# Kernel tuning notes

Hardware: AMD Instinct MI355X
Metric: run time of the kernel (lower is better)

Reference implementation:

```python
import jax, jax.numpy as jnp
import numpy as np

B, S, HID, NH = 2, 2048, 1024, 16
HD = HID // NH  # head_dim = 64


def setup_inputs() -> dict:
    key = jax.random.key(0)
    ks = jax.random.split(key, 9)
    init = 0.02
    return {
        "x": jax.random.normal(ks[0], (B, S, HID), dtype=jnp.float32),
        "Wq": jax.random.normal(ks[1], (HID, HID), dtype=jnp.float32) * init,
        "bq": jnp.zeros((HID,), dtype=jnp.float32),
        "Wk": jax.random.normal(ks[2], (HID, HID), dtype=jnp.float32) * init,
        "bk": jnp.zeros((HID,), dtype=jnp.float32),
        "Wv": jax.random.normal(ks[3], (HID, HID), dtype=jnp.float32) * init,
        "bv": jnp.zeros((HID,), dtype=jnp.float32),
        "Wo": jax.random.normal(ks[4], (HID, HID), dtype=jnp.float32) * init,
        "bo": jnp.zeros((HID,), dtype=jnp.float32),
    }


def _split_heads(t):
    # [B, S, HID] -> [B, NH, S, HD]
    return t.reshape(B, S, NH, HD).transpose(0, 2, 1, 3)


def reference(x, Wq, bq, Wk, bk, Wv, bv, Wo, bo):
    q = _split_heads(x @ Wq.T + bq)
    k = _split_heads(x @ Wk.T + bk)
    v = _split_heads(x @ Wv.T + bv)

    # Faithful to source: scores = QK^T / (head_dim ** -0.5) == QK^T * sqrt(head_dim)
    inv_scale = jnp.asarray(HD ** (-0.5), dtype=x.dtype)
    scores = jnp.einsum("bhqd,bhkd->bhqk", q, k) / inv_scale

    causal_mask = jnp.triu(jnp.ones((S, S), dtype=bool), k=1)  # True above diagonal
    scores = jnp.where(causal_mask, jnp.asarray(-jnp.inf, dtype=scores.dtype), scores)
    attn = jax.nn.softmax(scores, axis=-1)  # dropout = identity (eval mode)

    ctx = jnp.einsum("bhqk,bhkd->bhqd", attn, v)
    ctx = ctx.transpose(0, 2, 1, 3).reshape(B, S, HID)
    out = ctx @ Wo.T + bo  # out_layer Linear; dropout = identity
    return out, attn
```

## Files before the change

### kernel.cpp

```cpp
#include <hip/hip_runtime.h>
#include <hip/hip_bf16.h>

#define BB   2
#define SS   2048
#define HID  1024
#define NH   16
#define HD   64
#define NEGS -30000.0f

typedef __bf16 bf16x8 __attribute__((ext_vector_type(8)));
typedef __bf16 bf16x4 __attribute__((ext_vector_type(4)));
typedef float  f32x4  __attribute__((ext_vector_type(4)));

static __device__ __forceinline__ f32x4 mfma_bf16(bf16x8 a, bf16x8 b, f32x4 c) {
    return __builtin_amdgcn_mfma_f32_16x16x32_bf16(a, b, c, 0, 0, 0);
}

static __device__ __forceinline__ void split_bf16(float f, __bf16* hp, __bf16* lp) {
    __bf16 h = (__bf16)f;
    *hp = h;
    *lp = (__bf16)(f - (float)h);
}

static __device__ __forceinline__ float clampf(float v, float lo, float hi) {
    return fminf(fmaxf(v, lo), hi);
}

static __device__ __forceinline__ void gll16(const __bf16* g, __bf16* l) {
    __builtin_amdgcn_global_load_lds((const void*)g, (void*)l, 16, 0, 0);
}

static __device__ __forceinline__ void barrier_lds() {
    asm volatile("s_waitcnt lgkmcnt(0)" ::: "memory");
    __builtin_amdgcn_sched_barrier(0);
    __builtin_amdgcn_s_barrier();
    __builtin_amdgcn_sched_barrier(0);
}

static __device__ __forceinline__ void barrier_vm4() {
    asm volatile("s_waitcnt vmcnt(4) lgkmcnt(0)" ::: "memory");
    __builtin_amdgcn_sched_barrier(0);
    __builtin_amdgcn_s_barrier();
    __builtin_amdgcn_sched_barrier(0);
}
static __device__ __forceinline__ void barrier_vm0() {
    asm volatile("s_waitcnt vmcnt(0) lgkmcnt(0)" ::: "memory");
    __builtin_amdgcn_sched_barrier(0);
    __builtin_amdgcn_s_barrier();
    __builtin_amdgcn_sched_barrier(0);
}

__global__ __launch_bounds__(256) void split_kernel(
    const float* __restrict__ x,
    const float* __restrict__ Wq, const float* __restrict__ Wk,
    const float* __restrict__ Wv, const float* __restrict__ Wo,
    __bf16* __restrict__ xh, __bf16* __restrict__ xl,
    __bf16* __restrict__ wqh, __bf16* __restrict__ wql,
    __bf16* __restrict__ wkh, __bf16* __restrict__ wkl,
    __bf16* __restrict__ wvh, __bf16* __restrict__ woh)
{
    const int bid = blockIdx.x;
    if (bid < 4096) {
        const int i4 = bid * 256 + threadIdx.x;
        const float4 v = ((const float4*)x)[i4];
        const float* p = (const float*)&v;
        bf16x4 h4, l4v;
#pragma unroll
        for (int j = 0; j < 4; j++) { __bf16 hh, ll; split_bf16(p[j], &hh, &ll); h4[j] = hh; l4v[j] = ll; }
        *(bf16x4*)&xh[(size_t)i4 * 4] = h4;
        *(bf16x4*)&xl[(size_t)i4 * 4] = l4v;
        return;
    }
    const int wb = bid - 4096;
    const int which = (wb >> 10) + 1;
    const int i4 = (wb & 1023) * 256 + threadIdx.x;
    const float* src = which == 1 ? Wq : which == 2 ? Wk : which == 3 ? Wv : Wo;
    const float sc = (which == 1) ? 8.0f : 1.0f;
    const float4 v = ((const float4*)src)[i4];
    const float* p = (const float*)&v;
    bf16x4 h4, l4v;
#pragma unroll
    for (int j = 0; j < 4; j++) { __bf16 hh, ll; split_bf16(p[j] * sc, &hh, &ll); h4[j] = hh; l4v[j] = ll; }
    if (which == 1)      { *(bf16x4*)&wqh[(size_t)i4 * 4] = h4; *(bf16x4*)&wql[(size_t)i4 * 4] = l4v; }
    else if (which == 2) { *(bf16x4*)&wkh[(size_t)i4 * 4] = h4; *(bf16x4*)&wkl[(size_t)i4 * 4] = l4v; }
    else if (which == 3) { *(bf16x4*)&wvh[(size_t)i4 * 4] = h4; }
    else                 { *(bf16x4*)&woh[(size_t)i4 * 4] = h4; }
}

__global__ __launch_bounds__(256) void qkv_kernel(
    const __bf16* __restrict__ xh, const __bf16* __restrict__ xl,
    const __bf16* __restrict__ wqh, const __bf16* __restrict__ wql,
    const __bf16* __restrict__ wkh, const __bf16* __restrict__ wkl,
    const __bf16* __restrict__ wvh,
    const float* __restrict__ bq, const float* __restrict__ bk, const float* __restrict__ bv,
    __bf16* __restrict__ qh, __bf16* __restrict__ ql,
    __bf16* __restrict__ kh, __bf16* __restrict__ kl,
    __bf16* __restrict__ vt)
{
    __shared__ __align__(16) __bf16 smem[32768];

    const int stream = blockIdx.x >> 3, ct = blockIdx.x & 7;
    const int t0 = blockIdx.y * 128, c0 = ct * 128;
    const bool qk = stream < 2;
    const __bf16* const Bhg = stream == 0 ? wqh : stream == 1 ? wkh : wvh;
    const __bf16* const Blg = stream == 0 ? wql : wkl;
    const float* const bias = stream == 0 ? bq : stream == 1 ? bk : bv;
    const float bscale = stream == 0 ? 8.0f : 1.0f;

    const int tid = threadIdx.x, wave = tid >> 6, lane = tid & 63;
    const int l16 = lane & 15, quad = lane >> 4;
    const int wr = wave >> 1, wc = wave & 1;

    const int ar0 = tid >> 2,         as0 = (tid & 3) ^ (ar0 & 3);
    const int ar1 = (256 + tid) >> 2, as1 = ((256 + tid) & 3) ^ (ar1 & 3);
    const size_t aoff0 = (size_t)(t0 + ar0) * HID + as0 * 8;
    const size_t aoff1 = (size_t)(t0 + ar1) * HID + as1 * 8;
    const size_t boff0 = (size_t)(c0 + ar0) * HID + as0 * 8;
    const size_t boff1 = (size_t)(c0 + ar1) * HID + as1 * 8;
    const int ld0 = wave << 9, ld1 = (4 + wave) << 9;

#define QKV_STAGE(b_, k0_) do {                                   \
        __bf16* s_ = smem + (b_) * 16384;                         \
        gll16(xh + aoff0 + (k0_), s_ + ld0);                      \
        gll16(xh + aoff1 + (k0_), s_ + ld1);                      \
        gll16(Bhg + boff0 + (k0_), s_ + 8192 + ld0);              \
        gll16(Bhg + boff1 + (k0_), s_ + 8192 + ld1);              \
        if (qk) {                                                 \
            gll16(xl + aoff0 + (k0_), s_ + 4096 + ld0);           \
            gll16(xl + aoff1 + (k0_), s_ + 4096 + ld1);           \
            gll16(Blg + boff0 + (k0_), s_ + 12288 + ld0);         \
            gll16(Blg + boff1 + (k0_), s_ + 12288 + ld1);         \
        }                                                         \
    } while (0)

    const f32x4 zero4 = {0.f, 0.f, 0.f, 0.f};
    f32x4 acc[4][4];
#pragma unroll
    for (int i = 0; i < 4; i++)
#pragma unroll
        for (int j = 0; j < 4; j++) acc[i][j] = zero4;

    QKV_STAGE(0, 0);
    for (int k0 = 0; k0 < HID; k0 += 32) {
        const int cur = (k0 >> 5) & 1;
        __syncthreads();
        if (k0 + 32 < HID) QKV_STAGE(cur ^ 1, k0 + 32);
        __bf16* const s_ = smem + cur * 16384;

        bf16x8 aH[4], aL[4], bHf[4], bLf[4];
#pragma unroll
        for (int mf = 0; mf < 4; mf++) {
            const int row = wr * 64 + mf * 16 + l16;
            const int off = row * 32 + ((quad ^ (row & 3)) << 3);
            aH[mf] = *(const bf16x8*)(s_ + off);
            if (qk) aL[mf] = *(const bf16x8*)(s_ + 4096 + off);
        }
#pragma unroll
        for (int nf = 0; nf < 4; nf++) {
            const int row = wc * 64 + nf * 16 + l16;
            const int off = row * 32 + ((quad ^ (row & 3)) << 3);
            bHf[nf] = *(const bf16x8*)(s_ + 8192 + off);
            if (qk) bLf[nf] = *(const bf16x8*)(s_ + 12288 + off);
        }
#pragma unroll
        for (int mf = 0; mf < 4; mf++)
#pragma unroll
            for (int nf = 0; nf < 4; nf++) {
                acc[mf][nf] = mfma_bf16(aH[mf], bHf[nf], acc[mf][nf]);
                if (qk) {
                    acc[mf][nf] = mfma_bf16(aH[mf], bLf[nf], acc[mf][nf]);
                    acc[mf][nf] = mfma_bf16(aL[mf], bHf[nf], acc[mf][nf]);
                }
            }
    }
#undef QKV_STAGE

    const int bidx = t0 >> 11;
    const int s0 = t0 & (SS - 1);

    if (qk) {
        __bf16* const Es = smem;
        __bf16* const hi_arr = stream == 0 ? qh : kh;
        __bf16* const lo_arr = stream == 0 ? ql : kl;
#pragma unroll
        for (int pass = 0; pass < 2; pass++) {
            __syncthreads();
#pragma unroll
            for (int nf = 0; nf < 4; nf++) {
                const int dcl = wc * 64 + nf * 16 + l16;
                const float bv_ = bias[c0 + dcl] * bscale;
#pragma unroll
                for (int mf = 0; mf < 4; mf++)
#pragma unroll
                    for (int r = 0; r < 4; r++) {
                        const int srl = wr * 64 + mf * 16 + quad * 4 + r;
                        const float v = clampf(acc[mf][nf][r] + bv_, -1e4f, 1e4f);
                        __bf16 hv, lv;
                        split_bf16(v, &hv, &lv);
                        Es[srl * 132 + dcl] = pass ? lv : hv;
                    }
            }
            __syncthreads();
            __bf16* const dst = pass ? lo_arr : hi_arr;
#pragma unroll
            for (int i = 0; i < 8; i++) {
                const int idx = tid + i * 256;
                const int row = idx >> 4, c16 = idx & 15;
                const int hh = (c0 >> 6) + (c16 >> 3);
                const int dd = (c16 & 7) * 8;
                const size_t o = ((size_t)(bidx * NH + hh) * SS + (s0 + row)) * HD + dd;
                *(uint4*)&dst[o] = *(const uint4*)&Es[row * 132 + c16 * 8];
            }
        }
    } else {
        __syncthreads();
        __bf16* const Vts = smem + wave * 4608;
#pragma unroll
        for (int nf = 0; nf < 4; nf++) {
            const int dloc = nf * 16 + l16;
            const float bv_ = bias[c0 + wc * 64 + dloc];
#pragma unroll
            for (int mf = 0; mf < 4; mf++)
#pragma unroll
                for (int r = 0; r < 4; r++)
                    Vts[dloc * 72 + mf * 16 + quad * 4 + r] =
                        (__bf16)clampf(acc[mf][nf][r] + bv_, -1e4f, 1e4f);
        }
        const int hh = (c0 + wc * 64) >> 6;
        const size_t vb = (size_t)(bidx * NH + hh) * HD * SS;
        const int sc0 = s0 + wr * 64;
#pragma unroll
        for (int j = 0; j < 8; j++) {
            const int idx = j * 64 + lane;
            const int d = idx >> 3, c8 = idx & 7;
            *(uint4*)&vt[vb + (size_t)d * SS + sc0 + c8 * 8] =
                *(const uint4*)&Vts[d * 72 + c8 * 8];
        }
    }
}

__global__ __launch_bounds__(512, 4) void attn_kernel(
    const __bf16* __restrict__ qh, const __bf16* __restrict__ ql,
    const __bf16* __restrict__ kh, const __bf16* __restrict__ kl,
    const __bf16* __restrict__ vt,
    float* __restrict__ attn, __bf16* __restrict__ ctx)
{
    __shared__ __align__(16) __bf16 Kh0[4096], Kl0[4096], Kh1[4096], Kl1[4096];
    __shared__ __align__(16) __bf16 Vt0[4096], Vt1[4096];
    __shared__ __align__(16) __bf16 Ps[128][72];

    const int bid  = blockIdx.x;
    const int half = bid >> 8;
    const int ii   = bid & 255;
    const int g    = ii & 7;
    const int bh   = g + 8 * ((ii >> 3) & 3);
    const int p    = ii >> 5;
    const int qt   = half ? p : (15 - p);
    const int nj   = 2 * qt + 2;
    const int b    = bh >> 4, h = bh & 15;

    const int tid  = threadIdx.x;
    const int wave = tid >> 6, lane = tid & 63;
    const int l16  = lane & 15, quad = lane >> 4;

    const int sr = tid >> 3, ssw = (tid & 7) ^ (sr & 7);
    const size_t kq = (size_t)sr * HD + ssw * 8;
    const size_t vq = (size_t)sr * SS + ssw * 8;
    const int ldw = wave << 9;

    const __bf16* const khp = kh + (size_t)bh * SS * HD;
    const __bf16* const klp = kl + (size_t)bh * SS * HD;
    const __bf16* const vtp = vt + (size_t)bh * HD * SS;

#define STAGE_K(j_, KH, KL) do {                                  \
        const __bf16* kg_ = khp + (size_t)(j_) * (64 * HD);       \
        const __bf16* lg_ = klp + (size_t)(j_) * (64 * HD);       \
        gll16(kg_ + kq, (KH) + ldw); gll16(lg_ + kq, (KL) + ldw); \
    } while (0)
#define STAGE_V(j_, VT) do {                                      \
        const __bf16* vg_ = vtp + (size_t)(j_) * 64;              \
        gll16(vg_ + vq, (VT) + ldw);                              \
    } while (0)

    const f32x4 zero4 = {0.f, 0.f, 0.f, 0.f};

    bf16x8 aHq[2], aLq[2];
    {
        const size_t qrow = ((size_t)bh * SS + qt * 128 + wave * 16 + l16) * HD;
#pragma unroll
        for (int ks = 0; ks < 2; ks++) {
            aHq[ks] = *(const bf16x8*)&qh[qrow + ks * 32 + quad * 8];
            aLq[ks] = *(const bf16x8*)&ql[qrow + ks * 32 + quad * 8];
        }
    }

    float m4[4], l4[4];
#pragma unroll
    for (int r = 0; r < 4; r++) { m4[r] = NEGS; l4[r] = 0.f; }

    STAGE_K(0, Kh0, Kl0);
    __syncthreads();

    for (int j = 0; j < nj; j++) {
        if (j) __syncthreads();
        if (j < nj - 1) {
            if (j & 1) STAGE_K(j + 1, Kh0, Kl0);
            else       STAGE_K(j + 1, Kh1, Kl1);
        }
        const __bf16* const Khc = (j & 1) ? Kh1 : Kh0;
        const __bf16* const Klc = (j & 1) ? Kl1 : Kl0;

        f32x4 sacc[4] = {zero4, zero4, zero4, zero4};
#pragma unroll
        for (int ks = 0; ks < 2; ks++)
#pragma unroll
            for (int c = 0; c < 4; c++) {
                const int krow = c * 16 + l16;
                const int ko = krow * 64 + (((ks * 4 + quad) ^ (krow & 7)) << 3);
                const bf16x8 bH = *(const bf16x8*)(Khc + ko);
                const bf16x8 bL = *(const bf16x8*)(Klc + ko);
                sacc[c] = mfma_bf16(aHq[ks], bH, sacc[c]);
                sacc[c] = mfma_bf16(aHq[ks], bL, sacc[c]);
                sacc[c] = mfma_bf16(aLq[ks], bH, sacc[c]);
            }
        if (j >= 2 * qt) {
            const int cb = j * 64, qr = qt * 128 + wave * 16 + quad * 4;
#pragma unroll
            for (int c = 0; c < 4; c++) {
                const int col = cb + c * 16 + l16;
#pragma unroll
                for (int r = 0; r < 4; r++)
                    if (col > qr + r) sacc[c][r] = NEGS;
            }
        }
#pragma unroll
        for (int r = 0; r < 4; r++) {
            const float mx = fmaxf(fmaxf(sacc[0][r], sacc[1][r]),
                                   fmaxf(sacc[2][r], sacc[3][r]));
            const float mn = fmaxf(m4[r], mx);
            l4[r] = l4[r] * __expf(m4[r] - mn)
                  + __expf(sacc[0][r] - mn) + __expf(sacc[1][r] - mn)
                  + __expf(sacc[2][r] - mn) + __expf(sacc[3][r] - mn);
            m4[r] = mn;
        }
    }

    float il[4];
#pragma unroll
    for (int r = 0; r < 4; r++) {
#pragma unroll
        for (int off = 1; off < 16; off <<= 1) {
            const float mo  = __shfl_xor(m4[r], off);
            const float lo_ = __shfl_xor(l4[r], off);
            const float mn  = fmaxf(m4[r], mo);
            l4[r] = l4[r] * __expf(m4[r] - mn) + lo_ * __expf(mo - mn);
            m4[r] = mn;
        }
        il[r] = (l4[r] > 0.f) ? (1.0f / l4[r]) : 0.f;
    }

    f32x4 cacc[4] = {zero4, zero4, zero4, zero4};

    __syncthreads();
    STAGE_K(0, Kh0, Kl0);
    STAGE_V(0, Vt0);

    for (int j = 0; j < nj; j++) {
        if (j == 0) barrier_vm0();
        else        barrier_vm4();
        if (j < nj - 1) {
            if (j & 1) { STAGE_K(j + 1, Kh0, Kl0); STAGE_V(j + 1, Vt0); }
            else       { STAGE_K(j + 1, Kh1, Kl1); STAGE_V(j + 1, Vt1); }
        }
        const __bf16* const Khc = (j & 1) ? Kh1 : Kh0;
        const __bf16* const Klc = (j & 1) ? Kl1 : Kl0;
        const __bf16* const Vtc = (j & 1) ? Vt1 : Vt0;

        f32x4 sacc[4] = {zero4, zero4, zero4, zero4};
#pragma unroll
        for (int ks = 0; ks < 2; ks++)
#pragma unroll
            for (int c = 0; c < 4; c++) {
                const int krow = c * 16 + l16;
                const int ko = krow * 64 + (((ks * 4 + quad) ^ (krow & 7)) << 3);
                const bf16x8 bH = *(const bf16x8*)(Khc + ko);
                const bf16x8 bL = *(const bf16x8*)(Klc + ko);
                sacc[c] = mfma_bf16(aHq[ks], bH, sacc[c]);
                sacc[c] = mfma_bf16(aHq[ks], bL, sacc[c]);
                sacc[c] = mfma_bf16(aLq[ks], bH, sacc[c]);
            }
        if (j >= 2 * qt) {
            const int cb = j * 64, qr = qt * 128 + wave * 16 + quad * 4;
#pragma unroll
            for (int c = 0; c < 4; c++) {
                const int col = cb + c * 16 + l16;
#pragma unroll
                for (int r = 0; r < 4; r++)
                    if (col > qr + r) sacc[c][r] = NEGS;
            }
        }
#pragma unroll
        for (int c = 0; c < 4; c++)
#pragma unroll
            for (int r = 0; r < 4; r++) {
                const float pv = clampf(__expf(sacc[c][r] - m4[r]) * il[r], 0.f, 1.f);
                Ps[wave * 16 + quad * 4 + r][c * 16 + l16] = (__bf16)pv;
            }
        barrier_lds();

#pragma unroll
        for (int i = 0; i < 2; i++) {
            const int idx = tid + i * 512;
            const int row = idx >> 3, c8 = idx & 7;
            const size_t o = ((size_t)bh * SS + qt * 128 + row) * SS + j * 64 + c8 * 8;
            __bf16 tmp[8];
            *(uint4*)tmp = *(const uint4*)&Ps[row][c8 * 8];
            float4 f0, f1;
            f0.x = (float)tmp[0]; f0.y = (float)tmp[1];
            f0.z = (float)tmp[2]; f0.w = (float)tmp[3];
            f1.x = (float)tmp[4]; f1.y = (float)tmp[5];
            f1.z = (float)tmp[6]; f1.w = (float)tmp[7];
            *(float4*)&attn[o]     = f0;
            *(float4*)&attn[o + 4] = f1;
        }
#pragma unroll
        for (int ks = 0; ks < 2; ks++) {
            const bf16x8 ap = *(const bf16x8*)&Ps[wave * 16 + l16][ks * 32 + quad * 8];
#pragma unroll
            for (int dt = 0; dt < 4; dt++) {
                const int vrow = dt * 16 + l16;
                const int vo = vrow * 64 + (((ks * 4 + quad) ^ (vrow & 7)) << 3);
                cacc[dt] = mfma_bf16(ap, *(const bf16x8*)(Vtc + vo), cacc[dt]);
            }
        }
    }

    const float4 zf4 = {0.f, 0.f, 0.f, 0.f};
    for (int j = nj; j < SS / 64; j++) {
#pragma unroll
        for (int i = 0; i < 4; i++) {
            const int idx = tid + i * 512;
            const int row = idx >> 4, c4 = idx & 15;
            const size_t o = ((size_t)bh * SS + qt * 128 + row) * SS + j * 64 + c4 * 4;
            *(float4*)&attn[o] = zf4;
        }
    }

    __syncthreads();
#pragma unroll
    for (int dt = 0; dt < 4; dt++) {
        const int d = dt * 16 + l16;
#pragma unroll
        for (int r = 0; r < 4; r++)
            Ps[wave * 16 + quad * 4 + r][d] =
                (__bf16)clampf(cacc[dt][r], -1e4f, 1e4f);
    }
    __syncthreads();
#pragma unroll
    for (int i = 0; i < 2; i++) {
        const int idx = tid + i * 512;
        const int row = idx >> 3, c8 = idx & 7;
        *(uint4*)&ctx[(size_t)(b * SS + qt * 128 + row) * HID + h * 64 + c8 * 8] =
            *(const uint4*)&Ps[row][c8 * 8];
    }
#undef STAGE_K
#undef STAGE_V
}

__global__ __launch_bounds__(256) void out_kernel(
    const __bf16* __restrict__ ctx, const __bf16* __restrict__ woh,
    const float* __restrict__ bo, float* __restrict__ out)
{
    __shared__ __align__(16) __bf16 smem[12288];

    const int o0 = blockIdx.x * 64;
    const int t0 = blockIdx.y * 128;

    const int tid = threadIdx.x, wave = tid >> 6, lane = tid & 63;
    const int l16 = lane & 15, quad = lane >> 4;
    const int wr = wave >> 1, wc = wave & 1;

    const int ar0 = tid >> 2,         as0 = (tid & 3) ^ (ar0 & 3);
    const int ar1 = (256 + tid) >> 2, as1 = ((256 + tid) & 3) ^ (ar1 & 3);
    const size_t aoff0 = (size_t)(t0 + ar0) * HID + as0 * 8;
    const size_t aoff1 = (size_t)(t0 + ar1) * HID + as1 * 8;
    const size_t boff  = (size_t)(o0 + ar0) * HID + as0 * 8;
    const int ld0 = wave << 9, ld1 = (4 + wave) << 9;

#define OUT_STAGE(b_, k0_) do {                                   \
        __bf16* s_ = smem + (b_) * 6144;                          \
        gll16(ctx + aoff0 + (k0_), s_ + ld0);                     \
        gll16(ctx + aoff1 + (k0_), s_ + ld1);                     \
        gll16(woh + boff + (k0_), s_ + 4096 + ld0);               \
    } while (0)

    const f32x4 zero4 = {0.f, 0.f, 0.f, 0.f};
    f32x4 acc[4][2];
#pragma unroll
    for (int i = 0; i < 4; i++)
#pragma unroll
        for (int j = 0; j < 2; j++) acc[i][j] = zero4;

    OUT_STAGE(0, 0);
    for (int k0 = 0; k0 < HID; k0 += 32) {
        const int cur = (k0 >> 5) & 1;
        __syncthreads();
        if (k0 + 32 < HID) OUT_STAGE(cur ^ 1, k0 + 32);
        __bf16* const s_ = smem + cur * 6144;

        bf16x8 aH[4], bHf[2];
#pragma unroll
        for (int mf = 0; mf < 4; mf++) {
            const int row = wr * 64 + mf * 16 + l16;
            aH[mf] = *(const bf16x8*)(s_ + row * 32 + ((quad ^ (row & 3)) << 3));
        }
#pragma unroll
        for (int nf = 0; nf < 2; nf++) {
            const int row = wc * 32 + nf * 16 + l16;
            bHf[nf] = *(const bf16x8*)(s_ + 4096 + row * 32 + ((quad ^ (row & 3)) << 3));
        }
#pragma unroll
        for (int mf = 0; mf < 4; mf++)
#pragma unroll
            for (int nf = 0; nf < 2; nf++)
                acc[mf][nf] = mfma_bf16(aH[mf], bHf[nf], acc[mf][nf]);
    }
#undef OUT_STAGE

#pragma unroll
    for (int nf = 0; nf < 2; nf++) {
        const int dcol = o0 + wc * 32 + nf * 16 + l16;
        const float bias = bo[dcol];
#pragma unroll
        for (int mf = 0; mf < 4; mf++)
#pragma unroll
            for (int r = 0; r < 4; r++) {
                const int t = t0 + wr * 64 + mf * 16 + quad * 4 + r;
                out[(size_t)t * HID + dcol] = clampf(acc[mf][nf][r] + bias, -1e4f, 1e4f);
            }
    }
}

extern "C" void kernel_launch(void* const* d_in, const int* in_sizes, int n_in,
                              void* d_out, int out_size, void* d_ws, size_t ws_size,
                              hipStream_t stream) {
    const float* x  = (const float*)d_in[0];
    const float* Wq = (const float*)d_in[1];
    const float* bq = (const float*)d_in[2];
    const float* Wk = (const float*)d_in[3];
    const float* bk = (const float*)d_in[4];
    const float* Wv = (const float*)d_in[5];
    const float* bv = (const float*)d_in[6];
    const float* Wo = (const float*)d_in[7];
    const float* bo = (const float*)d_in[8];

    float* out  = (float*)d_out;
    float* attn = out + (size_t)BB * SS * HID;

    const size_t NQ = (size_t)BB * NH * SS * HD;
    const size_t NW = (size_t)HID * HID;
    __bf16* ws  = (__bf16*)d_ws;
    __bf16* qh  = ws;
    __bf16* ql  = ws + NQ;
    __bf16* kh  = ws + 2 * NQ;
    __bf16* kl  = ws + 3 * NQ;
    __bf16* vt  = ws + 4 * NQ;
    __bf16* xh  = ws + 5 * NQ;
    __bf16* xl  = ws + 6 * NQ;
    __bf16* wqh = ws + 7 * NQ;
    __bf16* wql = wqh + NW;
    __bf16* wkh = wqh + 2 * NW;
    __bf16* wkl = wqh + 3 * NW;
    __bf16* wvh = wqh + 4 * NW;
    __bf16* woh = wqh + 5 * NW;
    __bf16* ctx = xh;

    split_kernel<<<dim3(8192), 256, 0, stream>>>(x, Wq, Wk, Wv, Wo,
                                                 xh, xl, wqh, wql, wkh, wkl, wvh, woh);
    qkv_kernel<<<dim3(24, 32), 256, 0, stream>>>(xh, xl, wqh, wql, wkh, wkl, wvh,
                                                 bq, bk, bv, qh, ql, kh, kl, vt);
    attn_kernel<<<dim3(512), 512, 0, stream>>>(qh, ql, kh, kl, vt, attn, ctx);
    out_kernel<<<dim3(16, 32), 256, 0, stream>>>(ctx, woh, bo, out);
}
```

Measured before the change: 723.7 us.

## Triple-buffer K stats pass, raise MFMA priority, nontemporal attn stores, reorder PV

The first softmax-statistics pass becomes a three-deep K pipeline that borrows the V buffers as a third slot and waits with counted vmcnt barriers instead of full syncthreads. s_setprio is raised around the MFMA blocks in every GEMM and attention loop. The P·V MFMAs now run before the attn tile is written out. Attn, zero-fill and out stores switch to nontemporal. Together these aim to overlap loads with compute and keep the large attn write stream out of the cache, but they add more in-flight loads and pressure on barrier ordering.

Measured after the change: 854.0 us. 1.18x slower.

```diff
diff --git a/kernel.cpp b/kernel.cpp
--- a/kernel.cpp
+++ b/kernel.cpp
@@ -37,14 +37,20 @@
     __builtin_amdgcn_sched_barrier(0);
 }
 
+static __device__ __forceinline__ void barrier_vm0() {
+    asm volatile("s_waitcnt vmcnt(0) lgkmcnt(0)" ::: "memory");
+    __builtin_amdgcn_sched_barrier(0);
+    __builtin_amdgcn_s_barrier();
+    __builtin_amdgcn_sched_barrier(0);
+}
+static __device__ __forceinline__ void barrier_vm2() {
+    asm volatile("s_waitcnt vmcnt(2) lgkmcnt(0)" ::: "memory");
+    __builtin_amdgcn_sched_barrier(0);
+    __builtin_amdgcn_s_barrier();
+    __builtin_amdgcn_sched_barrier(0);
+}
 static __device__ __forceinline__ void barrier_vm4() {
     asm volatile("s_waitcnt vmcnt(4) lgkmcnt(0)" ::: "memory");
-    __builtin_amdgcn_sched_barrier(0);
-    __builtin_amdgcn_s_barrier();
-    __builtin_amdgcn_sched_barrier(0);
-}
-static __device__ __forceinline__ void barrier_vm0() {
-    asm volatile("s_waitcnt vmcnt(0) lgkmcnt(0)" ::: "memory");
     __builtin_amdgcn_sched_barrier(0);
     __builtin_amdgcn_s_barrier();
     __builtin_amdgcn_sched_barrier(0);
@@ -162,6 +168,7 @@
             bHf[nf] = *(const bf16x8*)(s_ + 8192 + off);
             if (qk) bLf[nf] = *(const bf16x8*)(s_ + 12288 + off);
         }
+        __builtin_amdgcn_s_setprio(1);
 #pragma unroll
         for (int mf = 0; mf < 4; mf++)
 #pragma unroll
@@ -172,6 +179,7 @@
                     acc[mf][nf] = mfma_bf16(aL[mf], bHf[nf], acc[mf][nf]);
                 }
             }
+        __builtin_amdgcn_s_setprio(0);
     }
 #undef QKV_STAGE
 
@@ -299,18 +307,22 @@
     for (int r = 0; r < 4; r++) { m4[r] = NEGS; l4[r] = 0.f; }
 
     STAGE_K(0, Kh0, Kl0);
-    __syncthreads();
+    STAGE_K(1, Kh1, Kl1);
 
     for (int j = 0; j < nj; j++) {
-        if (j) __syncthreads();
-        if (j < nj - 1) {
-            if (j & 1) STAGE_K(j + 1, Kh0, Kl0);
-            else       STAGE_K(j + 1, Kh1, Kl1);
-        }
-        const __bf16* const Khc = (j & 1) ? Kh1 : Kh0;
-        const __bf16* const Klc = (j & 1) ? Kl1 : Kl0;
+        const int bi = j % 3;
+        if (j + 1 < nj) barrier_vm2(); else barrier_vm0();
+        if (j + 2 < nj) {
+            const int st = bi == 0 ? 2 : bi - 1;
+            __bf16* const KHs = st == 0 ? Kh0 : (st == 1 ? Kh1 : Vt0);
+            __bf16* const KLs = st == 0 ? Kl0 : (st == 1 ? Kl1 : Vt1);
+            STAGE_K(j + 2, KHs, KLs);
+        }
+        const __bf16* const Khc = bi == 0 ? Kh0 : (bi == 1 ? Kh1 : Vt0);
+        const __bf16* const Klc = bi == 0 ? Kl0 : (bi == 1 ? Kl1 : Vt1);
 
         f32x4 sacc[4] = {zero4, zero4, zero4, zero4};
+        __builtin_amdgcn_s_setprio(1);
 #pragma unroll
         for (int ks = 0; ks < 2; ks++)
 #pragma unroll
@@ -323,6 +335,7 @@
                 sacc[c] = mfma_bf16(aHq[ks], bL, sacc[c]);
                 sacc[c] = mfma_bf16(aLq[ks], bH, sacc[c]);
             }
+        __builtin_amdgcn_s_setprio(0);
         if (j >= 2 * qt) {
             const int cb = j * 64, qr = qt * 128 + wave * 16 + quad * 4;
 #pragma unroll
@@ -377,6 +390,7 @@
         const __bf16* const Vtc = (j & 1) ? Vt1 : Vt0;
 
         f32x4 sacc[4] = {zero4, zero4, zero4, zero4};
+        __builtin_amdgcn_s_setprio(1);
 #pragma unroll
         for (int ks = 0; ks < 2; ks++)
 #pragma unroll
@@ -389,6 +403,7 @@
                 sacc[c] = mfma_bf16(aHq[ks], bL, sacc[c]);
                 sacc[c] = mfma_bf16(aLq[ks], bH, sacc[c]);
             }
+        __builtin_amdgcn_s_setprio(0);
         if (j >= 2 * qt) {
             const int cb = j * 64, qr = qt * 128 + wave * 16 + quad * 4;
 #pragma unroll
@@ -407,6 +422,19 @@
                 Ps[wave * 16 + quad * 4 + r][c * 16 + l16] = (__bf16)pv;
             }
         barrier_lds();
+
+        __builtin_amdgcn_s_setprio(1);
+#pragma unroll
+        for (int ks = 0; ks < 2; ks++) {
+            const bf16x8 ap = *(const bf16x8*)&Ps[wave * 16 + l16][ks * 32 + quad * 8];
+#pragma unroll
+            for (int dt = 0; dt < 4; dt++) {
+                const int vrow = dt * 16 + l16;
+                const int vo = vrow * 64 + (((ks * 4 + quad) ^ (vrow & 7)) << 3);
+                cacc[dt] = mfma_bf16(ap, *(const bf16x8*)(Vtc + vo), cacc[dt]);
+            }
+        }
+        __builtin_amdgcn_s_setprio(0);
 
 #pragma unroll
         for (int i = 0; i < 2; i++) {
@@ -415,34 +443,24 @@
             const size_t o = ((size_t)bh * SS + qt * 128 + row) * SS + j * 64 + c8 * 8;
             __bf16 tmp[8];
             *(uint4*)tmp = *(const uint4*)&Ps[row][c8 * 8];
-            float4 f0, f1;
-            f0.x = (float)tmp[0]; f0.y = (float)tmp[1];
-            f0.z = (float)tmp[2]; f0.w = (float)tmp[3];
-            f1.x = (float)tmp[4]; f1.y = (float)tmp[5];
-            f1.z = (float)tmp[6]; f1.w = (float)tmp[7];
-            *(float4*)&attn[o]     = f0;
-            *(float4*)&attn[o + 4] = f1;
-        }
-#pragma unroll
-        for (int ks = 0; ks < 2; ks++) {
-            const bf16x8 ap = *(const bf16x8*)&Ps[wave * 16 + l16][ks * 32 + quad * 8];
-#pragma unroll
-            for (int dt = 0; dt < 4; dt++) {
-                const int vrow = dt * 16 + l16;
-                const int vo = vrow * 64 + (((ks * 4 + quad) ^ (vrow & 7)) << 3);
-                cacc[dt] = mfma_bf16(ap, *(const bf16x8*)(Vtc + vo), cacc[dt]);
-            }
-        }
-    }
-
-    const float4 zf4 = {0.f, 0.f, 0.f, 0.f};
+            f32x4 f0, f1;
+            f0[0] = (float)tmp[0]; f0[1] = (float)tmp[1];
+            f0[2] = (float)tmp[2]; f0[3] = (float)tmp[3];
+            f1[0] = (float)tmp[4]; f1[1] = (float)tmp[5];
+            f1[2] = (float)tmp[6]; f1[3] = (float)tmp[7];
+            __builtin_nontemporal_store(f0, (f32x4*)&attn[o]);
+            __builtin_nontemporal_store(f1, (f32x4*)&attn[o + 4]);
+        }
+    }
+
+    const f32x4 zf4 = {0.f, 0.f, 0.f, 0.f};
     for (int j = nj; j < SS / 64; j++) {
 #pragma unroll
         for (int i = 0; i < 4; i++) {
             const int idx = tid + i * 512;
             const int row = idx >> 4, c4 = idx & 15;
             const size_t o = ((size_t)bh * SS + qt * 128 + row) * SS + j * 64 + c4 * 4;
-            *(float4*)&attn[o] = zf4;
+            __builtin_nontemporal_store(zf4, (f32x4*)&attn[o]);
         }
     }
 
@@ -519,11 +537,13 @@
             const int row = wc * 32 + nf * 16 + l16;
             bHf[nf] = *(const bf16x8*)(s_ + 4096 + row * 32 + ((quad ^ (row & 3)) << 3));
         }
+        __builtin_amdgcn_s_setprio(1);
 #pragma unroll
         for (int mf = 0; mf < 4; mf++)
 #pragma unroll
             for (int nf = 0; nf < 2; nf++)
                 acc[mf][nf] = mfma_bf16(aH[mf], bHf[nf], acc[mf][nf]);
+        __builtin_amdgcn_s_setprio(0);
     }
 #undef OUT_STAGE
 
@@ -536,7 +556,8 @@
 #pragma unroll
             for (int r = 0; r < 4; r++) {
                 const int t = t0 + wr * 64 + mf * 16 + quad * 4 + r;
-                out[(size_t)t * HID + dcol] = clampf(acc[mf][nf][r] + bias, -1e4f, 1e4f);
+                __builtin_nontemporal_store(clampf(acc[mf][nf][r] + bias, -1e4f, 1e4f),
+                                            &out[(size_t)t * HID + dcol]);
             }
     }
 }
```
